# Kernel optimization log

Hardware: AMD Instinct MI355X
Metric: run time of the kernel (lower is better)

## Reference

```python
import jax, jax.numpy as jnp
import numpy as np

B, N, IN_DIM = 256, 300, 1280
DIM, DEPTH, HEADS = 256, 2, 4
DIM_HEAD = DIM // HEADS            # 64
NB_FEAT = int(DIM_HEAD * np.log(DIM_HEAD))  # 266, lucidrains default
FF_HIDDEN = 4 * DIM
LN_EPS = 1e-5
KERNEL_EPS = 1e-4


def _orthogonal_random_matrix(nb_rows, nb_cols, rng):
    # gaussian orthogonal random matrix, scaling=0 (chi-norm multipliers)
    blocks = []
    full = nb_rows // nb_cols
    for _ in range(full):
        q, _ = np.linalg.qr(rng.standard_normal((nb_cols, nb_cols)))
        blocks.append(q.T)
    rem = nb_rows - full * nb_cols
    if rem:
        q, _ = np.linalg.qr(rng.standard_normal((nb_cols, nb_cols)))
        blocks.append(q.T[:rem])
    mat = np.concatenate(blocks, 0)
    mult = np.linalg.norm(rng.standard_normal((nb_rows, nb_cols)), axis=1)
    return (mult[:, None] * mat).astype(np.float32)


def setup_inputs() -> dict:
    key = jax.random.key(0)
    ks = jax.random.split(key, 24)
    s = 0.02
    rng = np.random.default_rng(0)
    proj = jnp.asarray(np.stack([_orthogonal_random_matrix(NB_FEAT, DIM_HEAD, rng)
                                 for _ in range(DEPTH)]))  # [L, M, dh]
    return {
        "x": jax.random.normal(ks[0], (B, N, IN_DIM), jnp.float32),
        "w_in": jax.random.normal(ks[1], (IN_DIM, DIM), jnp.float32) * s,
        "b_in": jnp.zeros((DIM,), jnp.float32),
        "proj": proj,
        "ln1_g": jnp.ones((DEPTH, DIM), jnp.float32),
        "ln1_b": jnp.zeros((DEPTH, DIM), jnp.float32),
        "wq": jax.random.normal(ks[2], (DEPTH, DIM, DIM), jnp.float32) * s,
        "wk": jax.random.normal(ks[3], (DEPTH, DIM, DIM), jnp.float32) * s,
        "wv": jax.random.normal(ks[4], (DEPTH, DIM, DIM), jnp.float32) * s,
        "wo": jax.random.normal(ks[5], (DEPTH, DIM, DIM), jnp.float32) * s,
        "bo": jnp.zeros((DEPTH, DIM), jnp.float32),
        "ln2_g": jnp.ones((DEPTH, DIM), jnp.float32),
        "ln2_b": jnp.zeros((DEPTH, DIM), jnp.float32),
        "w1": jax.random.normal(ks[6], (DEPTH, DIM, FF_HIDDEN), jnp.float32) * s,
        "b1": jnp.zeros((DEPTH, FF_HIDDEN), jnp.float32),
        "w2": jax.random.normal(ks[7], (DEPTH, FF_HIDDEN, DIM), jnp.float32) * s,
        "b2": jnp.zeros((DEPTH, DIM), jnp.float32),
        "hln_g": jnp.ones((DIM,), jnp.float32),
        "hln_b": jnp.zeros((DIM,), jnp.float32),
        "wh1": jax.random.normal(ks[8], (DIM, 128), jnp.float32) * s,
        "bh1": jnp.zeros((128,), jnp.float32),
        "wh2": jax.random.normal(ks[9], (128, 1), jnp.float32) * s,
        "bh2": jnp.zeros((1,), jnp.float32),
    }


def _layernorm(x, g, b):
    mu = jnp.mean(x, -1, keepdims=True)
    var = jnp.mean(jnp.square(x - mu), -1, keepdims=True)
    return (x - mu) * jax.lax.rsqrt(var + LN_EPS) * g + b


def _softmax_kernel(data, proj, is_query):
    # data: [b,h,n,dh], proj: [m,dh] -> features [b,h,n,m] (FAVOR+ positive softmax kernel)
    norm = DIM_HEAD ** -0.25
    ratio = proj.shape[0] ** -0.5
    dd = jnp.einsum('bhnd,md->bhnm', data * norm, proj)
    diag = 0.5 * jnp.sum(jnp.square(data), -1) * (norm ** 2)  # [b,h,n]
    if is_query:
        stab = jnp.max(dd, axis=-1, keepdims=True)
    else:
        stab = jnp.max(dd, axis=(-2, -1), keepdims=True)
    return ratio * (jnp.exp(dd - diag[..., None] - stab) + KERNEL_EPS)


def _linear_attention(q, k, v, proj):
    # non-causal FAVOR+: O(n*m*d) instead of O(n^2*d)
    qp = _softmax_kernel(q, proj, True)    # [b,h,n,m]
    kp = _softmax_kernel(k, proj, False)   # [b,h,n,m]
    d_inv = 1.0 / jnp.einsum('bhnm,bhm->bhn', qp, jnp.sum(kp, axis=-2))
    context = jnp.einsum('bhnm,bhnd->bhmd', kp, v)
    return jnp.einsum('bhnm,bhmd->bhnd', qp, context) * d_inv[..., None]


def reference(x, w_in, b_in, proj, ln1_g, ln1_b, wq, wk, wv, wo, bo,
              ln2_g, ln2_b, w1, b1, w2, b2, hln_g, hln_b, wh1, bh1, wh2, bh2):
    h = x @ w_in + b_in                                   # [B,N,DIM]
    for l in range(DEPTH):
        # --- pre-norm FAVOR+ self-attention ---
        y = _layernorm(h, ln1_g[l], ln1_b[l])
        q = (y @ wq[l]).reshape(B, N, HEADS, DIM_HEAD).transpose(0, 2, 1, 3)
        k = (y @ wk[l]).reshape(B, N, HEADS, DIM_HEAD).transpose(0, 2, 1, 3)
        v = (y @ wv[l]).reshape(B, N, HEADS, DIM_HEAD).transpose(0, 2, 1, 3)
        o = _linear_attention(q, k, v, proj[l])
        o = o.transpose(0, 2, 1, 3).reshape(B, N, DIM)
        h = h + (o @ wo[l] + bo[l])
        # --- pre-norm FFN (GELU, mult=4) ---
        y = _layernorm(h, ln2_g[l], ln2_b[l])
        h = h + (jax.nn.gelu(y @ w1[l] + b1[l]) @ w2[l] + b2[l])
    pooled = jnp.mean(h, axis=1)                          # [B,DIM]
    z = _layernorm(pooled, hln_g, hln_b)
    z = jax.nn.relu(z @ wh1 + bh1)
    return jax.nn.sigmoid(z @ wh2 + bh2)                  # [B,1]
```

## Files before the change

kernel.cpp:

```cpp
#include <hip/hip_runtime.h>
#include <hip/hip_bf16.h>


#define MF 266
#define NSEQ 300
#define DIMC 256
#define NORM_QK 0.3535533905932738f
#define KEPS 1e-4f

typedef __attribute__((ext_vector_type(8))) short bf16x8;
typedef __attribute__((ext_vector_type(4))) float f32x4;

#define MFMA16(a, b, c) __builtin_amdgcn_mfma_f32_16x16x32_bf16((a), (b), (c), 0, 0, 0)

__device__ __forceinline__ float bfbits2f(ushort u) {
  return __uint_as_float(((unsigned int)u) << 16);
}
__device__ __forceinline__ ushort f2us(float f) {
  __hip_bfloat16 b = __float2bfloat16(f);
  return *(ushort*)&b;
}
__device__ __forceinline__ float sq8(uint4 u) {
  float s = 0.f;
  const unsigned int uu[4] = {u.x, u.y, u.z, u.w};
#pragma unroll
  for (int i = 0; i < 4; i++) {
    const float a = bfbits2f((ushort)(uu[i] & 0xffff));
    const float b = bfbits2f((ushort)(uu[i] >> 16));
    s += a * a + b * b;
  }
  return s;
}
__device__ __forceinline__ void gld16(const void* g, void* l) {
  __builtin_amdgcn_global_load_lds(
      (const __attribute__((address_space(1))) unsigned int*)g,
      (__attribute__((address_space(3))) unsigned int*)l, 16, 0, 0);
}
__device__ __forceinline__ float fast_gelu(float x) {
  const float t = 0.7978845608028654f * (x + 0.044715f * x * x * x);
  const float e = __expf(2.0f * fabsf(t));
  float th = 1.0f - 2.0f / (e + 1.0f);
  th = (t < 0.0f) ? -th : th;
  return 0.5f * x * (1.0f + th);
}

template<int EPI, int OUTBF, int AF32>
__global__ __launch_bounds__(256) void gemm_mfma(
    const ushort* __restrict__ A, const float* __restrict__ Af,
    const ushort* __restrict__ BT,
    const float* __restrict__ bias, const float* __restrict__ R,
    float* __restrict__ Cf, __hip_bfloat16* __restrict__ Cb,
    ushort* __restrict__ Cq, int M, int N, int K)
{
  __shared__ ushort As[128][32];
  __shared__ ushort Bs[128][32];
  const int tid = threadIdx.x;
  const int row0 = blockIdx.y << 7, col0 = blockIdx.x << 7;
  const int w = tid >> 6, lane = tid & 63;
  const int wm = (w >> 1) << 6, wn = (w & 1) << 6;
  const int r = lane & 15, quad = lane >> 4;
  const int sr = tid >> 2, sc = (tid & 3) << 3;
  f32x4 acc[4][4];
#pragma unroll
  for (int i = 0; i < 4; i++)
#pragma unroll
    for (int j = 0; j < 4; j++) acc[i][j] = (f32x4){0.f, 0.f, 0.f, 0.f};
  const ushort* ap0 = A + (size_t)(row0 + sr) * K + sc;
  const ushort* ap1 = A + (size_t)(row0 + sr + 64) * K + sc;
  const float*  af0 = Af + (size_t)(row0 + sr) * K + sc;
  const float*  af1 = Af + (size_t)(row0 + sr + 64) * K + sc;
  const ushort* bp0 = BT + (size_t)(col0 + sr) * K + sc;
  const ushort* bp1 = BT + (size_t)(col0 + sr + 64) * K + sc;
  for (int k0 = 0; k0 < K; k0 += 32) {
    if (AF32) {
      const float4 u0 = *(const float4*)(af0 + k0);
      const float4 u1 = *(const float4*)(af0 + k0 + 4);
      const float4 u2 = *(const float4*)(af1 + k0);
      const float4 u3 = *(const float4*)(af1 + k0 + 4);
      ushort4 p0, p1, p2, p3;
      p0.x=f2us(u0.x); p0.y=f2us(u0.y); p0.z=f2us(u0.z); p0.w=f2us(u0.w);
      p1.x=f2us(u1.x); p1.y=f2us(u1.y); p1.z=f2us(u1.z); p1.w=f2us(u1.w);
      p2.x=f2us(u2.x); p2.y=f2us(u2.y); p2.z=f2us(u2.z); p2.w=f2us(u2.w);
      p3.x=f2us(u3.x); p3.y=f2us(u3.y); p3.z=f2us(u3.z); p3.w=f2us(u3.w);
      *(ushort4*)&As[sr][sc]      = p0;
      *(ushort4*)&As[sr][sc+4]    = p1;
      *(ushort4*)&As[sr+64][sc]   = p2;
      *(ushort4*)&As[sr+64][sc+4] = p3;
    } else {
      gld16(ap0 + k0, &As[sr][sc]);
      gld16(ap1 + k0, &As[sr + 64][sc]);
    }
    gld16(bp0 + k0, &Bs[sr][sc]);
    gld16(bp1 + k0, &Bs[sr + 64][sc]);
    __syncthreads();
    bf16x8 af[4], bfv[4];
#pragma unroll
    for (int i = 0; i < 4; i++) af[i]  = *(const bf16x8*)&As[wm + i*16 + r][quad << 3];
#pragma unroll
    for (int i = 0; i < 4; i++) bfv[i] = *(const bf16x8*)&Bs[wn + i*16 + r][quad << 3];
#pragma unroll
    for (int mi = 0; mi < 4; mi++)
#pragma unroll
      for (int ni = 0; ni < 4; ni++)
        acc[mi][ni] = MFMA16(af[mi], bfv[ni], acc[mi][ni]);
    __syncthreads();
  }
#pragma unroll
  for (int mi = 0; mi < 4; mi++) {
    const int rowb = row0 + wm + mi*16 + (quad << 2);
#pragma unroll
    for (int ni = 0; ni < 4; ni++) {
      const int col = col0 + wn + ni*16 + r;
      if (EPI == 4) {
        const int tsel = col >> 8, hd = col & 255, hh = hd >> 6, d = hd & 63;
        const float sc_ = (tsel == 2) ? 1.f : NORM_QK;
#pragma unroll
        for (int j = 0; j < 4; j++) {
          const int rowj = rowb + j;
          const int bq = rowj / 300, nq = rowj - bq * 300;
          Cq[(((size_t)tsel * 1024 + (bq << 2) + hh) * 300 + nq) * 64 + d] =
              f2us(acc[mi][ni][j] * sc_);
        }
      } else {
        const float bv = bias[col];
#pragma unroll
        for (int j = 0; j < 4; j++) {
          const size_t off = (size_t)(rowb + j) * N + col;
          float vv = acc[mi][ni][j] + bv;
          if (EPI == 1) vv += R[off];
          if (OUTBF) Cb[off] = __float2bfloat16(vv);
          else       Cf[off] = vv;
        }
      }
    }
  }
}

__global__ __launch_bounds__(256) void pack_ffn(
    const ushort* __restrict__ w1T, const ushort* __restrict__ w2T,
    ushort* __restrict__ W1P, ushort* __restrict__ W2P)
{
  const int c = blockIdx.x * 256 + threadIdx.x;
  const int ci = c & 32767;
  const int l = ci & 63, g = ci >> 6;
  const int r = l & 15, q = l >> 4;
  size_t src;
  ushort* dst;
  if (c < 32768) {
    const int nc = g >> 6, w = (g >> 3) & 7, ks = g & 7;
    src = (size_t)(nc*128 + w*16 + r) * 256 + ks*32 + q*8;
    dst = W1P + (size_t)ci * 8;
    *(uint4*)dst = *(const uint4*)(w1T + src);
  } else {
    const int nc = g >> 6, w = (g >> 3) & 7, kq = (g >> 1) & 3, jn = g & 1;
    src = (size_t)(w*32 + jn*16 + r) * 1024 + nc*128 + kq*32 + q*8;
    dst = W2P + (size_t)ci * 8;
    *(uint4*)dst = *(const uint4*)(w2T + src);
  }
}

__global__ __launch_bounds__(512, 6) void ffn_fused_kernel(
    float* __restrict__ h, const ushort* __restrict__ W1P,
    const float* __restrict__ b1, const ushort* __restrict__ W2P,
    const float* __restrict__ b2, const float* __restrict__ lng,
    const float* __restrict__ lnb)
{
  __shared__ ushort Ys[64][264];
  __shared__ ushort Hs[64][136];
  const int tid = threadIdx.x, w = tid >> 6, lane = tid & 63;
  const int r = lane & 15, quad = lane >> 4;
  const int row0 = blockIdx.x << 6;

  {
    const int rl = lane >> 3, c8 = lane & 7;
    const int row = (w << 3) + rl;
    const float4* h4 = (const float4*)(h + (size_t)(row0 + row) * DIMC);
    float4 v[8];
    float s = 0.f;
#pragma unroll
    for (int g = 0; g < 8; g++) {
      v[g] = h4[g*8 + c8];
      s += v[g].x + v[g].y + v[g].z + v[g].w;
    }
    s += __shfl_xor(s, 1); s += __shfl_xor(s, 2); s += __shfl_xor(s, 4);
    const float mu = s * (1.0f/256.0f);
    float var = 0.f;
#pragma unroll
    for (int g = 0; g < 8; g++) {
      const float a=v[g].x-mu, b=v[g].y-mu, c=v[g].z-mu, d=v[g].w-mu;
      var += a*a + b*b + c*c + d*d;
    }
    var += __shfl_xor(var, 1); var += __shfl_xor(var, 2); var += __shfl_xor(var, 4);
    const float rstd = rsqrtf(var * (1.0f/256.0f) + 1e-5f);
#pragma unroll
    for (int g = 0; g < 8; g++) {
      const int col = (g*8 + c8) << 2;
      const float4 gg = *(const float4*)(lng + col);
      const float4 bb = *(const float4*)(lnb + col);
      ushort4 o;
      o.x = f2us((v[g].x - mu) * rstd * gg.x + bb.x);
      o.y = f2us((v[g].y - mu) * rstd * gg.y + bb.y);
      o.z = f2us((v[g].z - mu) * rstd * gg.z + bb.z);
      o.w = f2us((v[g].w - mu) * rstd * gg.w + bb.w);
      *(ushort4*)&Ys[row][col] = o;
    }
  }
  __syncthreads();

  f32x4 oacc[4][2];
#pragma unroll
  for (int i = 0; i < 4; i++)
#pragma unroll
    for (int j = 0; j < 2; j++) oacc[i][j] = (f32x4){0.f, 0.f, 0.f, 0.f};

  for (int nc = 0; nc < 8; nc++) {
    f32x4 hacc[4];
#pragma unroll
    for (int i = 0; i < 4; i++) hacc[i] = (f32x4){0.f, 0.f, 0.f, 0.f};
    const ushort* w1p = W1P + ((size_t)((nc*8 + w) * 8) * 64 + lane) * 8;
#pragma unroll
    for (int ks = 0; ks < 8; ks++) {
      const bf16x8 a = *(const bf16x8*)(w1p + ks * 512);
#pragma unroll
      for (int mj = 0; mj < 4; mj++) {
        const bf16x8 y = *(const bf16x8*)&Ys[mj*16 + r][ks*32 + (quad << 3)];
        hacc[mj] = MFMA16(a, y, hacc[mj]);
      }
    }
    const int khb = (w << 4) + (quad << 2);
    const float4 bv = *(const float4*)(b1 + nc*128 + khb);
#pragma unroll
    for (int mj = 0; mj < 4; mj++) {
      ushort4 hv;
      hv.x = f2us(fast_gelu(hacc[mj][0] + bv.x));
      hv.y = f2us(fast_gelu(hacc[mj][1] + bv.y));
      hv.z = f2us(fast_gelu(hacc[mj][2] + bv.z));
      hv.w = f2us(fast_gelu(hacc[mj][3] + bv.w));
      *(ushort4*)&Hs[mj*16 + r][khb] = hv;
    }
    __syncthreads();
    const ushort* w2p = W2P + ((size_t)((nc*8 + w) * 8) * 64 + lane) * 8;
#pragma unroll
    for (int kq = 0; kq < 4; kq++) {
      bf16x8 hf[4];
#pragma unroll
      for (int mi = 0; mi < 4; mi++)
        hf[mi] = *(const bf16x8*)&Hs[mi*16 + r][kq*32 + (quad << 3)];
#pragma unroll
      for (int jn = 0; jn < 2; jn++) {
        const bf16x8 bb = *(const bf16x8*)(w2p + (kq*2 + jn) * 512);
#pragma unroll
        for (int mi = 0; mi < 4; mi++)
          oacc[mi][jn] = MFMA16(hf[mi], bb, oacc[mi][jn]);
      }
    }
    __syncthreads();
  }

#pragma unroll
  for (int mi = 0; mi < 4; mi++) {
    const int mbase = row0 + mi*16 + (quad << 2);
#pragma unroll
    for (int jn = 0; jn < 2; jn++) {
      const int n = (w << 5) + jn*16 + r;
      const float b2v = b2[n];
#pragma unroll
      for (int jj = 0; jj < 4; jj++) {
        float* hp = h + (size_t)(mbase + jj) * DIMC + n;
        *hp += oacc[mi][jn][jj] + b2v;
      }
    }
  }
}

__global__ __launch_bounds__(256) void cast_bf16_kernel(
    const float* __restrict__ in, ushort* __restrict__ out, int n4)
{
  const int i = blockIdx.x * 256 + threadIdx.x;
  if (i >= n4) return;
  const float4 v = ((const float4*)in)[i];
  ushort4 rr;
  rr.x = f2us(v.x); rr.y = f2us(v.y); rr.z = f2us(v.z); rr.w = f2us(v.w);
  ((ushort4*)out)[i] = rr;
}

struct TSeg { const float* src; ushort* dst; int R; int C; int base; };
struct TTab { TSeg s[13]; };
__global__ __launch_bounds__(256) void tcast_all(TTab tab) {
  __shared__ float t[32][33];
  const int bid = blockIdx.x;
  int si = 0;
#pragma unroll
  for (int i = 1; i < 13; i++) if (bid >= tab.s[i].base) si = i;
  const float* src = tab.s[si].src;
  ushort* dst = tab.s[si].dst;
  const int R = tab.s[si].R, C = tab.s[si].C;
  const int local = bid - tab.s[si].base;
  const int cw = C >> 5;
  const int c0 = (local % cw) << 5, r0 = (local / cw) << 5;
  const int tx = threadIdx.x & 31, ty = threadIdx.x >> 5;
#pragma unroll
  for (int i = 0; i < 32; i += 8)
    t[ty + i][tx] = src[(size_t)(r0 + ty + i) * C + c0 + tx];
  __syncthreads();
#pragma unroll
  for (int i = 0; i < 32; i += 8)
    dst[(size_t)(c0 + ty + i) * R + r0 + tx] = f2us(t[tx][ty + i]);
}

__global__ __launch_bounds__(256) void ln_kernel(
    const float* __restrict__ x, const float* __restrict__ g,
    const float* __restrict__ b, __hip_bfloat16* __restrict__ y)
{
  const int wid = threadIdx.x >> 6, lane = threadIdx.x & 63;
  const int row = blockIdx.x * 4 + wid;
  const float* xr = x + (size_t)row * DIMC;
  float v[4];
  float s = 0.f;
#pragma unroll
  for (int i = 0; i < 4; i++) { v[i] = xr[lane + 64*i]; s += v[i]; }
#pragma unroll
  for (int off = 32; off; off >>= 1) s += __shfl_xor(s, off);
  const float mu = s * (1.0f/256.0f);
  float var = 0.f;
#pragma unroll
  for (int i = 0; i < 4; i++) { const float d = v[i] - mu; var += d*d; }
#pragma unroll
  for (int off = 32; off; off >>= 1) var += __shfl_xor(var, off);
  const float rstd = rsqrtf(var * (1.0f/256.0f) + 1e-5f);
  __hip_bfloat16* yr = y + (size_t)row * DIMC;
#pragma unroll
  for (int i = 0; i < 4; i++) {
    const int c = lane + 64*i;
    yr[c] = __float2bfloat16((v[i] - mu) * rstd * g[c] + b[c]);
  }
}

__global__ __launch_bounds__(512) void favor_fused_kernel(
    const ushort* __restrict__ qn_all, const ushort* __restrict__ kn_all,
    const ushort* __restrict__ v_all, const ushort* __restrict__ projb,
    ushort* __restrict__ Ob)
{
  __shared__ __align__(16) uint8_t smem[151424];
  ushort (*kn_s)[72]      = (ushort(*)[72])(smem);
  ushort (*vT_s)[328]     = (ushort(*)[328])(smem + 46080);
  ushort (*proj_s)[72]    = (ushort(*)[72])(smem + 88064);
  ushort (*kpT_s)[40]     = (ushort(*)[40])(smem + 127232);
  ushort (*qp_s)[16][72]  = (ushort(*)[16][72])(smem + 127232);
  float* diag_s = (float*)(smem + 148992);
  float* ksum_s = (float*)(smem + 150272);
  float* red_s  = (float*)(smem + 151360);

  const int tid = threadIdx.x, w = tid >> 6, lane = tid & 63;
  const int bh = blockIdx.x;
  const int b = bh >> 2, h = bh & 3;
  const int r = lane & 15, quad = lane >> 4;
  const int rl = lane >> 3, c8 = lane & 7;

  {
    const ushort* knb = kn_all + (size_t)bh * 19200;
    for (int row = w*8 + rl; row < 320; row += 64) {
      uint4 u = {0u,0u,0u,0u};
      if (row < 300) u = *(const uint4*)(knb + row*64 + c8*8);
      *(uint4*)&kn_s[row][c8*8] = u;
      float s = sq8(u);
      s += __shfl_xor(s, 1); s += __shfl_xor(s, 2); s += __shfl_xor(s, 4);
      if (c8 == 0) diag_s[row] = 0.5f * s;
    }
    const ushort* vb = v_all + (size_t)bh * 19200;
    for (int row = w*8 + rl; row < 328; row += 64) {
      uint4 u = {0u,0u,0u,0u};
      if (row < 300) u = *(const uint4*)(vb + row*64 + c8*8);
      const unsigned int uu[4] = {u.x, u.y, u.z, u.w};
#pragma unroll
      for (int p = 0; p < 4; p++) {
        vT_s[c8*8 + 2*p    ][row] = (ushort)(uu[p] & 0xffff);
        vT_s[c8*8 + 2*p + 1][row] = (ushort)(uu[p] >> 16);
      }
    }
    for (int row = w*8 + rl; row < 272; row += 64) {
      uint4 u = {0u,0u,0u,0u};
      if (row < 266) u = *(const uint4*)(projb + row*64 + c8*8);
      *(uint4*)&proj_s[row][c8*8] = u;
    }
  }
  __syncthreads();

  f32x4 cacc[9];
#pragma unroll
  for (int i = 0; i < 9; i++) cacc[i] = (f32x4){0.f,0.f,0.f,0.f};
  float ksum_acc = 0.f;
  float stab = -3.0e38f;

  for (int c = 0; c < 10; c++) {
    f32x4 ddreg[5];
    float cmax = -3.0e38f;
#pragma unroll
    for (int ii = 0; ii < 5; ii++) {
      const int t = w + ii*8;
      if (t < 34) {
        const int tm = t >> 1, tn = c*2 + (t & 1);
        const bf16x8 a0 = *(const bf16x8*)&proj_s[tm*16 + r][quad*8];
        const bf16x8 a1 = *(const bf16x8*)&proj_s[tm*16 + r][32 + quad*8];
        const bf16x8 b0 = *(const bf16x8*)&kn_s[tn*16 + r][quad*8];
        const bf16x8 b1 = *(const bf16x8*)&kn_s[tn*16 + r][32 + quad*8];
        f32x4 acc = (f32x4){0.f,0.f,0.f,0.f};
        acc = MFMA16(a0, b0, acc);
        acc = MFMA16(a1, b1, acc);
        ddreg[ii] = acc;
        const int n = tn*16 + r;
        if (n < 300) {
#pragma unroll
          for (int j = 0; j < 4; j++) {
            const int m = tm*16 + quad*4 + j;
            if (m < 266) cmax = fmaxf(cmax, acc[j]);
          }
        }
      }
    }
#pragma unroll
    for (int off = 32; off; off >>= 1) cmax = fmaxf(cmax, __shfl_xor(cmax, off));
    if (lane == 0) red_s[w] = cmax;
    __syncthreads();
    float bmax = red_s[0];
#pragma unroll
    for (int i = 1; i < 8; i++) bmax = fmaxf(bmax, red_s[i]);
    const float stab_new = fmaxf(stab, bmax);
    const float alpha = __expf(stab - stab_new);
    stab = stab_new;
    ksum_acc *= alpha;
#pragma unroll
    for (int i = 0; i < 9; i++)
#pragma unroll
      for (int j = 0; j < 4; j++) cacc[i][j] *= alpha;
#pragma unroll
    for (int ii = 0; ii < 5; ii++) {
      const int t = w + ii*8;
      if (t < 34) {
        const int tm = t >> 1, tnl = t & 1, tn = c*2 + tnl;
        const int n = tn*16 + r;
        const float dgn = diag_s[n];
#pragma unroll
        for (int j = 0; j < 4; j++) {
          const int m = tm*16 + quad*4 + j;
          float kp = 0.f;
          if (n < 300 && m < 266) kp = __expf(ddreg[ii][j] - dgn - stab) + KEPS;
          kpT_s[m][tnl*16 + r] = f2us(kp);
        }
      }
    }
    __syncthreads();
    if (tid < 272) {
      float rs = 0.f;
#pragma unroll
      for (int kk = 0; kk < 4; kk++) {
        const uint4 u = *(const uint4*)&kpT_s[tid][kk*8];
        const unsigned int uu[4] = {u.x, u.y, u.z, u.w};
#pragma unroll
        for (int p = 0; p < 4; p++)
          rs += bfbits2f((ushort)(uu[p] & 0xffff)) + bfbits2f((ushort)(uu[p] >> 16));
      }
      ksum_acc += rs;
    }
#pragma unroll
    for (int ii = 0; ii < 9; ii++) {
      const int t2 = w + ii*8;
      if (t2 < 68) {
        const int tm = t2 >> 2, td = t2 & 3;
        const bf16x8 aa = *(const bf16x8*)&kpT_s[tm*16 + r][quad*8];
        const bf16x8 bb = *(const bf16x8*)&vT_s[td*16 + r][c*32 + quad*8];
        cacc[ii] = MFMA16(aa, bb, cacc[ii]);
      }
    }
    __syncthreads();
  }

  if (tid < 272) ksum_s[tid] = ksum_acc;
#pragma unroll
  for (int ii = 0; ii < 9; ii++) {
    const int t2 = w + ii*8;
    if (t2 < 68) {
      const int tm = t2 >> 2, td = t2 & 3;
#pragma unroll
      for (int j = 0; j < 4; j++) {
        const int m = tm*16 + quad*4 + j;
        vT_s[td*16 + r][m] = f2us(cacc[ii][j]);
      }
    }
  }
  {
    const ushort* qb = qn_all + (size_t)bh * 19200;
    for (int row = w*8 + rl; row < 320; row += 64) {
      uint4 u = {0u,0u,0u,0u};
      if (row < 300) u = *(const uint4*)(qb + row*64 + c8*8);
      *(uint4*)&kn_s[row][c8*8] = u;
      float s = sq8(u);
      s += __shfl_xor(s, 1); s += __shfl_xor(s, 2); s += __shfl_xor(s, 4);
      if (c8 == 0) diag_s[row] = 0.5f * s;
    }
  }
  __syncthreads();

  for (int t = w; t < 19; t += 8) {
    const bf16x8 a0 = *(const bf16x8*)&kn_s[t*16 + r][quad*8];
    const bf16x8 a1 = *(const bf16x8*)&kn_s[t*16 + r][32 + quad*8];
    f32x4 dd[17];
#pragma unroll
    for (int tm = 0; tm < 17; tm++) {
      const bf16x8 b0 = *(const bf16x8*)&proj_s[tm*16 + r][quad*8];
      const bf16x8 b1 = *(const bf16x8*)&proj_s[tm*16 + r][32 + quad*8];
      f32x4 acc = (f32x4){0.f,0.f,0.f,0.f};
      acc = MFMA16(a0, b0, acc);
      acc = MFMA16(a1, b1, acc);
      dd[tm] = acc;
    }
    float mxj[4] = {-3.0e38f, -3.0e38f, -3.0e38f, -3.0e38f};
#pragma unroll
    for (int tm = 0; tm < 17; tm++) {
      if (tm*16 + r < 266) {
#pragma unroll
        for (int j = 0; j < 4; j++) mxj[j] = fmaxf(mxj[j], dd[tm][j]);
      }
    }
#pragma unroll
    for (int off = 1; off < 16; off <<= 1)
#pragma unroll
      for (int j = 0; j < 4; j++) mxj[j] = fmaxf(mxj[j], __shfl_xor(mxj[j], off));
    float dg[4];
#pragma unroll
    for (int j = 0; j < 4; j++) dg[j] = diag_s[t*16 + quad*4 + j];
    float den[4] = {0.f, 0.f, 0.f, 0.f};
#pragma unroll
    for (int tm = 0; tm < 17; tm++) {
      const float ks = ksum_s[tm*16 + r];
      const bool mval = (tm*16 + r < 266);
#pragma unroll
      for (int j = 0; j < 4; j++) {
        const int n = t*16 + quad*4 + j;
        float qp = 0.f;
        if (mval && n < 300) qp = __expf(dd[tm][j] - dg[j] - mxj[j]) + KEPS;
        dd[tm][j] = qp;
        den[j] += qp * ks;
      }
    }
#pragma unroll
    for (int off = 1; off < 16; off <<= 1)
#pragma unroll
      for (int j = 0; j < 4; j++) den[j] += __shfl_xor(den[j], off);
    float dinv[4];
#pragma unroll
    for (int j = 0; j < 4; j++) dinv[j] = 1.0f / den[j];

    f32x4 oacc[4];
#pragma unroll
    for (int td = 0; td < 4; td++) oacc[td] = (f32x4){0.f,0.f,0.f,0.f};
#pragma unroll
    for (int g = 0; g < 5; g++) {
#pragma unroll
      for (int tt = 0; tt < 4; tt++) {
        const int tm = g*4 + tt;
#pragma unroll
        for (int j = 0; j < 4; j++) {
          const ushort us = (tm <= 16) ? f2us(dd[tm][j]) : (ushort)0;
          qp_s[w][quad*4 + j][tt*16 + r] = us;
        }
      }
#pragma unroll
      for (int s = 0; s < 2; s++) {
        const bf16x8 aa = *(const bf16x8*)&qp_s[w][r][s*32 + quad*8];
#pragma unroll
        for (int td = 0; td < 4; td++) {
          const bf16x8 bb = *(const bf16x8*)&vT_s[td*16 + r][g*64 + s*32 + quad*8];
          oacc[td] = MFMA16(aa, bb, oacc[td]);
        }
      }
    }
#pragma unroll
    for (int td = 0; td < 4; td++) {
#pragma unroll
      for (int j = 0; j < 4; j++) {
        const int n = t*16 + quad*4 + j;
        if (n < 300)
          Ob[((size_t)b*300 + n)*256 + h*64 + td*16 + r] = f2us(oacc[td][j] * dinv[j]);
      }
    }
  }
}

__global__ __launch_bounds__(256) void head_kernel(
    const float* __restrict__ h, const float* __restrict__ hg,
    const float* __restrict__ hb, const float* __restrict__ wh1,
    const float* __restrict__ bh1, const float* __restrict__ wh2,
    const float* __restrict__ bh2, float* __restrict__ out)
{
  __shared__ float z_s[256];
  __shared__ float hid_s[128];
  __shared__ float red_s[4];
  const int b = blockIdx.x, tid = threadIdx.x;
  const float* hb_ = h + (size_t)b * NSEQ * DIMC;
  float s = 0.f;
  for (int n = 0; n < NSEQ; n++) s += hb_[(size_t)n * DIMC + tid];
  s *= (1.0f / 300.0f);
  float t1 = s;
#pragma unroll
  for (int off = 32; off; off >>= 1) t1 += __shfl_xor(t1, off);
  if ((tid & 63) == 0) red_s[tid >> 6] = t1;
  __syncthreads();
  const float mu = (red_s[0] + red_s[1] + red_s[2] + red_s[3]) * (1.0f/256.0f);
  __syncthreads();
  const float d = s - mu;
  float vv = d * d;
#pragma unroll
  for (int off = 32; off; off >>= 1) vv += __shfl_xor(vv, off);
  if ((tid & 63) == 0) red_s[tid >> 6] = vv;
  __syncthreads();
  const float var = (red_s[0] + red_s[1] + red_s[2] + red_s[3]) * (1.0f/256.0f);
  z_s[tid] = d * rsqrtf(var + 1e-5f) * hg[tid] + hb[tid];
  __syncthreads();
  if (tid < 128) {
    float acc = bh1[tid];
    for (int dd = 0; dd < 256; dd++) acc += z_s[dd] * wh1[dd * 128 + tid];
    hid_s[tid] = fmaxf(acc, 0.f);
  }
  __syncthreads();
  if (tid < 64) {
    float acc = hid_s[tid] * wh2[tid] + hid_s[tid + 64] * wh2[tid + 64];
#pragma unroll
    for (int off = 32; off; off >>= 1) acc += __shfl_xor(acc, off);
    if (tid == 0) {
      const float val = acc + bh2[0];
      out[b] = 1.0f / (1.0f + __expf(-val));
    }
  }
}

extern "C" void kernel_launch(void* const* d_in, const int* in_sizes, int n_in,
                              void* d_out, int out_size, void* d_ws, size_t ws_size,
                              hipStream_t stream) {
  const float* x    = (const float*)d_in[0];
  const float* w_in = (const float*)d_in[1];
  const float* b_in = (const float*)d_in[2];
  const float* proj = (const float*)d_in[3];
  const float* ln1g = (const float*)d_in[4];
  const float* ln1b = (const float*)d_in[5];
  const float* wq   = (const float*)d_in[6];
  const float* wk   = (const float*)d_in[7];
  const float* wv   = (const float*)d_in[8];
  const float* wo   = (const float*)d_in[9];
  const float* bo   = (const float*)d_in[10];
  const float* ln2g = (const float*)d_in[11];
  const float* ln2b = (const float*)d_in[12];
  const float* w1   = (const float*)d_in[13];
  const float* b1   = (const float*)d_in[14];
  const float* w2   = (const float*)d_in[15];
  const float* b2   = (const float*)d_in[16];
  const float* hg   = (const float*)d_in[17];
  const float* hbp  = (const float*)d_in[18];
  const float* wh1  = (const float*)d_in[19];
  const float* bh1  = (const float*)d_in[20];
  const float* wh2  = (const float*)d_in[21];
  const float* bh2  = (const float*)d_in[22];

  uint8_t* base = (uint8_t*)d_ws;
  float*  h     = (float*)(base);
  ushort* yb    = (ushort*)(base + 78643200);
  ushort* qkv   = (ushort*)(base + 117964800);
  ushort* ob    = (ushort*)(base + 235929600);
  ushort* wbuf  = (ushort*)(base + 275251200);
  ushort* projb = (ushort*)(base + 279052288);
  ushort* qb = qkv;
  ushort* kb = qkv + 19660800;
  ushort* vb = qkv + 39321600;
  ushort* scr = qkv;

  ushort* w_inT = wbuf;
  ushort* wT0   = wbuf + 327680;

  cast_bf16_kernel<<<34, 256, 0, stream>>>(proj, projb, 8512);
  TTab tab;
  int nb = 0;
  {
    int idx = 0, basem = 0;
    auto seg = [&](const float* s, ushort* d, int R, int C) {
      tab.s[idx] = TSeg{s, d, R, C, basem};
      basem += (R >> 5) * (C >> 5);
      idx++;
    };
    seg(w_in, w_inT, 1280, 256);
    for (int l = 0; l < 2; l++) {
      ushort* wl = wT0 + (size_t)l * 786432;
      seg(wq + (size_t)l*65536,  wl,          256, 256);
      seg(wk + (size_t)l*65536,  wl + 65536,  256, 256);
      seg(wv + (size_t)l*65536,  wl + 131072, 256, 256);
      seg(wo + (size_t)l*65536,  wl + 196608, 256, 256);
      seg(w1 + (size_t)l*262144, scr + (size_t)l*524288,          256, 1024);
      seg(w2 + (size_t)l*262144, scr + (size_t)l*524288 + 262144, 1024, 256);
    }
    nb = basem;
  }
  tcast_all<<<nb, 256, 0, stream>>>(tab);
  for (int l = 0; l < 2; l++) {
    ushort* wl = wT0 + (size_t)l * 786432;
    pack_ffn<<<256, 256, 0, stream>>>(
        scr + (size_t)l*524288, scr + (size_t)l*524288 + 262144,
        wl + 262144, wl + 524288);
  }

  gemm_mfma<0,0,1><<<dim3(2, 600), 256, 0, stream>>>(
      nullptr, x, w_inT, b_in, nullptr, h, nullptr, nullptr, 76800, 256, 1280);

  for (int l = 0; l < 2; l++) {
    ushort* wl = wT0 + (size_t)l * 786432;
    ushort* projL = projb + (size_t)l * 17024;
    ln_kernel<<<19200, 256, 0, stream>>>(h, ln1g + l*256, ln1b + l*256, (__hip_bfloat16*)yb);
    gemm_mfma<4,0,0><<<dim3(6, 600), 256, 0, stream>>>(
        yb, nullptr, wl, nullptr, nullptr, nullptr, nullptr, qkv, 76800, 768, 256);
    favor_fused_kernel<<<1024, 512, 0, stream>>>(qb, kb, vb, projL, ob);
    gemm_mfma<1,0,0><<<dim3(2, 600), 256, 0, stream>>>(
        ob, nullptr, wl + 196608, bo + l*256, h, h, nullptr, nullptr, 76800, 256, 256);
    ffn_fused_kernel<<<1200, 512, 0, stream>>>(
        h, wl + 262144, b1 + (size_t)l*1024, wl + 524288, b2 + (size_t)l*256,
        ln2g + l*256, ln2b + l*256);
  }
  head_kernel<<<256, 256, 0, stream>>>(h, hg, hbp, wh1, bh1, wh2, bh2, (float*)d_out);
}
```

Before: 1.595 ms.

## Fuse attention output projection and residual into the fused FFN kernel

The separate output-projection GEMM (ob @ wo + bo + residual) now runs inside the FFN kernel. Each block loads its 64 rows of attention output into shared memory and multiplies them against a pre-packed wo layout with MFMA. It then adds the bias and residual, computes LayerNorm statistics through a cross-wave shared reduction, writes h back, and feeds the normalized bf16 rows straight into the FFN. This removes one kernel launch and a global round trip of h between the two stages. The cost is extra per-block work and possible register pressure, and variance is now computed as E[x²]−mu², which is less numerically robust.

```diff
diff --git a/kernel.cpp b/kernel.cpp
--- a/kernel.cpp
+++ b/kernel.cpp
@@ -138,71 +138,119 @@
 
 __global__ __launch_bounds__(256) void pack_ffn(
     const ushort* __restrict__ w1T, const ushort* __restrict__ w2T,
-    ushort* __restrict__ W1P, ushort* __restrict__ W2P)
+    const ushort* __restrict__ woT,
+    ushort* __restrict__ W1P, ushort* __restrict__ W2P,
+    ushort* __restrict__ WOP)
 {
   const int c = blockIdx.x * 256 + threadIdx.x;
-  const int ci = c & 32767;
-  const int l = ci & 63, g = ci >> 6;
-  const int r = l & 15, q = l >> 4;
-  size_t src;
-  ushort* dst;
   if (c < 32768) {
+    const int l = c & 63, g = c >> 6;
+    const int r = l & 15, q = l >> 4;
     const int nc = g >> 6, w = (g >> 3) & 7, ks = g & 7;
-    src = (size_t)(nc*128 + w*16 + r) * 256 + ks*32 + q*8;
-    dst = W1P + (size_t)ci * 8;
-    *(uint4*)dst = *(const uint4*)(w1T + src);
+    *(uint4*)(W1P + (size_t)c * 8) =
+        *(const uint4*)(w1T + (size_t)(nc*128 + w*16 + r) * 256 + ks*32 + q*8);
+  } else if (c < 65536) {
+    const int ci = c - 32768;
+    const int l = ci & 63, g = ci >> 6;
+    const int r = l & 15, q = l >> 4;
+    const int nc = g >> 6, w = (g >> 3) & 7, kq = (g >> 1) & 3, jn = g & 1;
+    *(uint4*)(W2P + (size_t)ci * 8) =
+        *(const uint4*)(w2T + (size_t)(w*32 + jn*16 + r) * 1024 + nc*128 + kq*32 + q*8);
   } else {
-    const int nc = g >> 6, w = (g >> 3) & 7, kq = (g >> 1) & 3, jn = g & 1;
-    src = (size_t)(w*32 + jn*16 + r) * 1024 + nc*128 + kq*32 + q*8;
-    dst = W2P + (size_t)ci * 8;
-    *(uint4*)dst = *(const uint4*)(w2T + src);
-  }
-}
-
-__global__ __launch_bounds__(512, 6) void ffn_fused_kernel(
-    float* __restrict__ h, const ushort* __restrict__ W1P,
-    const float* __restrict__ b1, const ushort* __restrict__ W2P,
-    const float* __restrict__ b2, const float* __restrict__ lng,
-    const float* __restrict__ lnb)
+    const int ci = c - 65536;
+    const int l = ci & 63, g = ci >> 6;
+    const int r = l & 15, q = l >> 4;
+    const int ks = g >> 4, nt = g & 15;
+    *(uint4*)(WOP + (size_t)ci * 8) =
+        *(const uint4*)(woT + (size_t)(nt*16 + r) * 256 + ks*32 + q*8);
+  }
+}
+
+__global__ __launch_bounds__(512, 6) void aoffn_kernel(
+    float* __restrict__ h, const ushort* __restrict__ ob,
+    const ushort* __restrict__ WOP, const float* __restrict__ bo,
+    const ushort* __restrict__ W1P, const float* __restrict__ b1,
+    const ushort* __restrict__ W2P, const float* __restrict__ b2,
+    const float* __restrict__ lng, const float* __restrict__ lnb)
 {
   __shared__ ushort Ys[64][264];
   __shared__ ushort Hs[64][136];
+  __shared__ float red1[64][2], red2[64][2];
   const int tid = threadIdx.x, w = tid >> 6, lane = tid & 63;
   const int r = lane & 15, quad = lane >> 4;
   const int row0 = blockIdx.x << 6;
 
   {
-    const int rl = lane >> 3, c8 = lane & 7;
-    const int row = (w << 3) + rl;
-    const float4* h4 = (const float4*)(h + (size_t)(row0 + row) * DIMC);
-    float4 v[8];
-    float s = 0.f;
-#pragma unroll
-    for (int g = 0; g < 8; g++) {
-      v[g] = h4[g*8 + c8];
-      s += v[g].x + v[g].y + v[g].z + v[g].w;
-    }
-    s += __shfl_xor(s, 1); s += __shfl_xor(s, 2); s += __shfl_xor(s, 4);
-    const float mu = s * (1.0f/256.0f);
-    float var = 0.f;
-#pragma unroll
-    for (int g = 0; g < 8; g++) {
-      const float a=v[g].x-mu, b=v[g].y-mu, c=v[g].z-mu, d=v[g].w-mu;
-      var += a*a + b*b + c*c + d*d;
-    }
-    var += __shfl_xor(var, 1); var += __shfl_xor(var, 2); var += __shfl_xor(var, 4);
-    const float rstd = rsqrtf(var * (1.0f/256.0f) + 1e-5f);
-#pragma unroll
-    for (int g = 0; g < 8; g++) {
-      const int col = (g*8 + c8) << 2;
-      const float4 gg = *(const float4*)(lng + col);
-      const float4 bb = *(const float4*)(lnb + col);
-      ushort4 o;
-      o.x = f2us((v[g].x - mu) * rstd * gg.x + bb.x);
-      o.y = f2us((v[g].y - mu) * rstd * gg.y + bb.y);
-      o.z = f2us((v[g].z - mu) * rstd * gg.z + bb.z);
-      o.w = f2us((v[g].w - mu) * rstd * gg.w + bb.w);
-      *(ushort4*)&Ys[row][col] = o;
+    const ushort* obp = ob + (size_t)row0 * DIMC;
+#pragma unroll
+    for (int p = 0; p < 4; p++) {
+      const int i = tid + p*512;
+      const int rr = i >> 5, cc = (i & 31) << 3;
+      *(uint4*)&Ys[rr][cc] = *(const uint4*)(obp + rr*DIMC + cc);
+    }
+  }
+  __syncthreads();
+
+  const int mt = w & 3, nh = w >> 2;
+  f32x4 wacc[8];
+#pragma unroll
+  for (int i = 0; i < 8; i++) wacc[i] = (f32x4){0.f, 0.f, 0.f, 0.f};
+  {
+    const ushort* wop = WOP + ((size_t)(nh*8) * 64 + lane) * 8;
+#pragma unroll
+    for (int ks = 0; ks < 8; ks++) {
+      const bf16x8 a = *(const bf16x8*)&Ys[mt*16 + r][ks*32 + (quad << 3)];
+#pragma unroll
+      for (int nt = 0; nt < 8; nt++) {
+        const bf16x8 bb = *(const bf16x8*)(wop + ((size_t)ks*16 + nt) * 512);
+        wacc[nt] = MFMA16(a, bb, wacc[nt]);
+      }
+    }
+  }
+  {
+    float s1[4] = {0.f,0.f,0.f,0.f}, s2[4] = {0.f,0.f,0.f,0.f};
+#pragma unroll
+    for (int nt = 0; nt < 8; nt++) {
+      const int col = (nh << 7) + nt*16 + r;
+      const float bv = bo[col];
+#pragma unroll
+      for (int j = 0; j < 4; j++) {
+        const int rowj = mt*16 + (quad << 2) + j;
+        const float hn = wacc[nt][j] + bv + h[(size_t)(row0 + rowj)*DIMC + col];
+        s1[j] += hn; s2[j] += hn*hn;
+      }
+    }
+#pragma unroll
+    for (int off = 1; off < 16; off <<= 1)
+#pragma unroll
+      for (int j = 0; j < 4; j++) {
+        s1[j] += __shfl_xor(s1[j], off);
+        s2[j] += __shfl_xor(s2[j], off);
+      }
+    if (r == 0) {
+#pragma unroll
+      for (int j = 0; j < 4; j++) {
+        const int rowj = mt*16 + (quad << 2) + j;
+        red1[rowj][nh] = s1[j];
+        red2[rowj][nh] = s2[j];
+      }
+    }
+  }
+  __syncthreads();
+  {
+#pragma unroll
+    for (int j = 0; j < 4; j++) {
+      const int rowj = mt*16 + (quad << 2) + j;
+      const float mu = (red1[rowj][0] + red1[rowj][1]) * (1.0f/256.0f);
+      const float e2 = (red2[rowj][0] + red2[rowj][1]) * (1.0f/256.0f);
+      const float rstd = rsqrtf(e2 - mu*mu + 1e-5f);
+#pragma unroll
+      for (int nt = 0; nt < 8; nt++) {
+        const int col = (nh << 7) + nt*16 + r;
+        const float hn = wacc[nt][j] + bo[col] + h[(size_t)(row0 + rowj)*DIMC + col];
+        h[(size_t)(row0 + rowj)*DIMC + col] = hn;
+        Ys[rowj][col] = f2us((hn - mu) * rstd * lng[col] + lnb[col]);
+      }
     }
   }
   __syncthreads();
@@ -668,6 +716,7 @@
   ushort* ob    = (ushort*)(base + 235929600);
   ushort* wbuf  = (ushort*)(base + 275251200);
   ushort* projb = (ushort*)(base + 279052288);
+  ushort* wopb  = (ushort*)(base + 279120384);
   ushort* qb = qkv;
   ushort* kb = qkv + 19660800;
   ushort* vb = qkv + 39321600;
@@ -701,9 +750,10 @@
   tcast_all<<<nb, 256, 0, stream>>>(tab);
   for (int l = 0; l < 2; l++) {
     ushort* wl = wT0 + (size_t)l * 786432;
-    pack_ffn<<<256, 256, 0, stream>>>(
+    pack_ffn<<<288, 256, 0, stream>>>(
         scr + (size_t)l*524288, scr + (size_t)l*524288 + 262144,
-        wl + 262144, wl + 524288);
+        wl + 196608,
+        wl + 262144, wl + 524288, wopb + (size_t)l*65536);
   }
 
   gemm_mfma<0,0,1><<<dim3(2, 600), 256, 0, stream>>>(
@@ -716,10 +766,9 @@
     gemm_mfma<4,0,0><<<dim3(6, 600), 256, 0, stream>>>(
         yb, nullptr, wl, nullptr, nullptr, nullptr, nullptr, qkv, 76800, 768, 256);
     favor_fused_kernel<<<1024, 512, 0, stream>>>(qb, kb, vb, projL, ob);
-    gemm_mfma<1,0,0><<<dim3(2, 600), 256, 0, stream>>>(
-        ob, nullptr, wl + 196608, bo + l*256, h, h, nullptr, nullptr, 76800, 256, 256);
-    ffn_fused_kernel<<<1200, 512, 0, stream>>>(
-        h, wl + 262144, b1 + (size_t)l*1024, wl + 524288, b2 + (size_t)l*256,
+    aoffn_kernel<<<1200, 512, 0, stream>>>(
+        h, ob, wopb + (size_t)l*65536, bo + l*256,
+        wl + 262144, b1 + (size_t)l*1024, wl + 524288, b2 + (size_t)l*256,
         ln2g + l*256, ln2b + l*256);
   }
   head_kernel<<<256, 256, 0, stream>>>(h, hg, hbp, wh1, bh1, wh2, bh2, (float*)d_out);
```

After: 1.638 ms. 1.03x slower.
